# Optimization experiments

Measured on AMD Instinct MI355X. Metric: run time of the kernel, lower is better.

Reference implementation:

```python
import jax, jax.numpy as jnp
import numpy as np

VOCAB = 32000
H = 256
B = 4
S = 512


def setup_inputs() -> dict:
    key = jax.random.key(0)
    ks = jax.random.split(key, 12)
    s = 1.0 / np.sqrt(H)
    inp = {
        "x": jax.random.randint(ks[0], (B, S), 0, VOCAB),
        "embed": jax.random.normal(ks[1], (VOCAB, H), jnp.float32) * 0.02,
        "Wi": jax.random.normal(ks[2], (H, H), jnp.float32) * s,   # i2h weight (in,out)
        "bi": jax.random.normal(ks[3], (H,), jnp.float32) * s,
        "Wh": jax.random.normal(ks[4], (H, H), jnp.float32) * s,   # h2h weight
        "bh": jax.random.normal(ks[5], (H,), jnp.float32) * s,
        "Wa": jax.random.normal(ks[6], (2 * H, H), jnp.float32) * s,  # attn_W (in=2H,out=H)
        "ba": jax.random.normal(ks[7], (H,), jnp.float32) * s,
        "va": jax.random.normal(ks[8], (H,), jnp.float32) * s,     # attn_v (no bias)
        "Wo": jax.random.normal(ks[9], (H, VOCAB), jnp.float32) * s,  # fc_out
        "bo": jax.random.normal(ks[10], (VOCAB,), jnp.float32) * s,
    }
    return inp


def _forward(x, embed, Wi, bi, Wh, bh, Wa, ba, va, Wo, bo):
    emb = embed[x]                               # [B,S,H]
    h0 = jnp.zeros((x.shape[0], H), emb.dtype)

    def step(h, e_t):
        h_new = jnp.tanh(e_t @ Wi + bi + h @ Wh + bh)
        return h_new, h_new

    _, hs = jax.lax.scan(step, h0, jnp.swapaxes(emb, 0, 1))  # [S,B,H]
    enc = jnp.swapaxes(hs, 0, 1)                 # [B,S,H] encoder states

    # Additive attention: energy(t,s) = tanh(W[ h_t ; h_s ] + b), score = v . energy
    Wq, Wk = Wa[:H], Wa[H:]
    q = enc @ Wq                                 # [B,S,H] (query = h_t half)
    k = enc @ Wk                                 # [B,S,H] (history half)
    energy = jnp.tanh(q[:, :, None, :] + k[:, None, :, :] + ba)  # [B,T,S,H]
    scores = jnp.einsum("btsh,h->bts", energy, va)

    seq = x.shape[1]
    causal = jnp.arange(seq)[None, :] < jnp.arange(seq)[:, None]  # [T,S]: s < t strictly
    weights = jax.nn.softmax(jnp.where(causal[None], scores, -1e9), axis=-1)
    ctx = jnp.einsum("bts,bsh->bth", weights, enc)               # [B,S,H]
    # t == 0: context = h_0 itself (no history)
    ctx = jnp.where((jnp.arange(seq) == 0)[None, :, None], enc[:, 0:1, :], ctx)

    out = (ctx + enc) @ Wo + bo                  # [B,S,V]
    return out, enc[:, -1, :]


def reference(x, embed, Wi, bi, Wh, bh, Wa, ba, va, Wo, bo):
    return _forward(x, embed, Wi, bi, Wh, bh, Wa, ba, va, Wo, bo)
```

## Files before the change

kernel.cpp:

```cpp
#include <hip/hip_runtime.h>
#include <hip/hip_bf16.h>
#include <hip/hip_fp16.h>

#define VOCAB 32000
#define H 256
#define B 4
#define S 512

typedef _Float16 f16x8 __attribute__((ext_vector_type(8)));
typedef short s16x8 __attribute__((ext_vector_type(8)));
typedef float f32x4 __attribute__((ext_vector_type(4)));

__device__ __forceinline__ float tanh_fast(float x) {
    float e = exp2f(x * 2.885390081777927f);
    return 1.0f - 2.0f * __builtin_amdgcn_rcpf(e + 1.0f);
}

__device__ __forceinline__ size_t fragIdx(int row, int h) {
    return ((size_t)((((row >> 4) * 8 + (h >> 5)) * 64) + ((h >> 3) & 3) * 16 + (row & 15)) << 3)
           + (h & 7);
}

__global__ __launch_bounds__(256) void k_wot(const float* __restrict__ Wo,
                                             ushort* __restrict__ WoTF) {
    __shared__ float tile[256][65];
    int n0 = blockIdx.x * 64;
    int tx = threadIdx.x & 63, ty = threadIdx.x >> 6;
#pragma unroll
    for (int i = 0; i < 64; ++i) {
        int k = i * 4 + ty;
        tile[k][tx] = Wo[(size_t)k * VOCAB + n0 + tx];
    }
    __syncthreads();
#pragma unroll
    for (int r = 0; r < 8; ++r) {
        int lin = threadIdx.x + 256 * r;
        int ll = lin & 15, lg = (lin >> 4) & 3, kk = (lin >> 6) & 7, nt = lin >> 9;
        int n = nt * 16 + ll;
        s16x8 v;
#pragma unroll
        for (int e = 0; e < 8; ++e) {
            __hip_bfloat16 b = __float2bfloat16(tile[kk * 32 + lg * 8 + e][n]);
            v[e] = *(short*)&b;
        }
        size_t unit = (size_t)(((n0 >> 4) + nt) * 8 + kk) * 64 + lg * 16 + ll;
        *(s16x8*)&WoTF[unit * 8] = v;
    }
}

__global__ void k_eprep(const int* __restrict__ x, const float* __restrict__ embed,
                        const float* __restrict__ Wi, const float* __restrict__ bi,
                        const float* __restrict__ bh, float* __restrict__ Ew) {
    int t = blockIdx.x, j = threadIdx.x;
    __shared__ float es[B][H];
    __shared__ int xs[B];
    if (j < B) xs[j] = x[j * S + t];
    __syncthreads();
    for (int b = 0; b < B; ++b) es[b][j] = embed[(size_t)xs[b] * H + j];
    float bias = bi[j] + bh[j];
    float a0 = bias, a1 = bias, a2 = bias, a3 = bias;
    __syncthreads();
    for (int i = 0; i < H; ++i) {
        float w = Wi[i * H + j];
        a0 += es[0][i] * w; a1 += es[1][i] * w;
        a2 += es[2][i] * w; a3 += es[3][i] * w;
    }
    f32x4 v; v[0] = a0; v[1] = a1; v[2] = a2; v[3] = a3;
    *(f32x4*)&Ew[(t * H + j) * 4] = v;
}

__global__ __launch_bounds__(256, 1) void k_rnn(const float* __restrict__ Ew,
                                                const float* __restrict__ Wh,
                                                _Float16* __restrict__ enc16,
                                                float* __restrict__ out_tail) {
    const int tid = threadIdx.x;
    const int w = tid >> 6;
    const int l = tid & 63;
    const int lg = l >> 4;
    const int ll = l & 15;

    __shared__ _Float16 hbuf[2][4][258];
    for (int idx = tid; idx < 2 * 4 * 258; idx += 256) (&hbuf[0][0][0])[idx] = (_Float16)0.f;

    f16x8 Bf[4][8];
#pragma unroll
    for (int nt = 0; nt < 4; ++nt) {
        int col = w * 64 + nt * 16 + ll;
#pragma unroll
        for (int kk = 0; kk < 8; ++kk) {
            int kb = kk * 32 + lg * 8;
            f16x8 v;
#pragma unroll
            for (int e = 0; e < 8; ++e) v[e] = (_Float16)Wh[(kb + e) * H + col];
            Bf[nt][kk] = v;
        }
    }
    __syncthreads();

    f32x4 eacc[2][4];
#pragma unroll
    for (int d = 0; d < 2; ++d)
#pragma unroll
        for (int nt = 0; nt < 4; ++nt) {
            int j = w * 64 + nt * 16 + ll;
            eacc[d][nt] = *(const f32x4*)&Ew[(d * H + j) * 4];
        }

    const int jcol = w * 64 + lg * 16 + ll;

    for (int t0 = 0; t0 < S; t0 += 2) {
#pragma unroll
        for (int u = 0; u < 2; ++u) {
            const int t = t0 + u;
            const int cur = u, nxt = u ^ 1;

            f16x8 Af[8];
#pragma unroll
            for (int kk = 0; kk < 8; ++kk)
                Af[kk] = *(const f16x8*)&hbuf[cur][l & 3][kk * 32 + lg * 8];

            f32x4 acc[4];
#pragma unroll
            for (int nt = 0; nt < 4; ++nt) acc[nt] = eacc[u][nt];

            {
                int tp = (t + 2 < S) ? t + 2 : S - 1;
#pragma unroll
                for (int nt = 0; nt < 4; ++nt) {
                    int j = w * 64 + nt * 16 + ll;
                    eacc[u][nt] = *(const f32x4*)&Ew[(tp * H + j) * 4];
                }
            }

#pragma unroll
            for (int kk = 0; kk < 8; ++kk)
#pragma unroll
                for (int nt = 0; nt < 4; ++nt)
                    acc[nt] = __builtin_amdgcn_mfma_f32_16x16x32_f16(Af[kk], Bf[nt][kk], acc[nt], 0, 0, 0);

            float v[4];
#pragma unroll
            for (int nt = 0; nt < 4; ++nt) {
                if (lg == nt) {
#pragma unroll
                    for (int r = 0; r < 4; ++r) v[r] = acc[nt][r];
                }
            }

            float hv[4];
#pragma unroll
            for (int r = 0; r < 4; ++r) hv[r] = tanh_fast(v[r]);

#pragma unroll
            for (int r = 0; r < 4; ++r) {
                _Float16 h16 = (_Float16)hv[r];
                hbuf[nxt][r][jcol] = h16;
                enc16[(r * S + t) * H + jcol] = h16;
            }
            if (t == S - 1) {
#pragma unroll
                for (int r = 0; r < 4; ++r) out_tail[r * H + jcol] = hv[r];
            }

            asm volatile("s_waitcnt lgkmcnt(0)" ::: "memory");
            __builtin_amdgcn_s_barrier();
            asm volatile("" ::: "memory");
        }
    }
}

__global__ void k_qk(const _Float16* __restrict__ enc16, const float* __restrict__ Wa,
                     const float* __restrict__ ba, float* __restrict__ q,
                     float* __restrict__ kT, ushort* __restrict__ encF) {
    int r0 = blockIdx.x * 8;
    int j = threadIdx.x;
    __shared__ float es[8][H];
#pragma unroll
    for (int r = 0; r < 8; ++r) es[r][j] = (float)enc16[(r0 + r) * H + j];
    __syncthreads();
    float aq[8] = {0, 0, 0, 0, 0, 0, 0, 0};
    float ak[8] = {0, 0, 0, 0, 0, 0, 0, 0};
    for (int i = 0; i < H; ++i) {
        float wq = Wa[i * H + j];
        float wk = Wa[(H + i) * H + j];
#pragma unroll
        for (int r = 0; r < 8; ++r) { aq[r] += es[r][i] * wq; ak[r] += es[r][i] * wk; }
    }
    float bav = ba[j];
#pragma unroll
    for (int r = 0; r < 8; ++r) {
        int row = r0 + r;
        int b = row >> 9, t = row & (S - 1);
        q[row * H + j] = aq[r];
        kT[((b * H + j) << 9) + t] = ak[r] + bav;
        _Float16 ev = (_Float16)es[r][j];
        size_t unit = (size_t)((b * 16 + (j >> 4)) * 16 + (t >> 5)) * 64 + ((t >> 3) & 3) * 16 + (j & 15);
        encF[unit * 8 + (t & 7)] = *(ushort*)&ev;
    }
}

__global__ void k_attn(const float* __restrict__ q, const float* __restrict__ kT,
                       const float* __restrict__ va, ushort* __restrict__ WgtF) {
    int bt = blockIdx.x;
    int b = bt >> 9, t = bt & (S - 1);
    int tid = threadIdx.x;
    if (t == 0) {
        for (int ss = tid; ss < S; ss += 256) {
            _Float16 hw = (_Float16)((ss == 0) ? 1.f : 0.f);
            size_t unit = (size_t)((b * 32 + (t >> 4)) * 16 + (ss >> 5)) * 64 + ((ss >> 3) & 3) * 16 + (t & 15);
            WgtF[unit * 8 + (ss & 7)] = *(ushort*)&hw;
        }
        return;
    }
    __shared__ float qs[H], vas[H], part[4][S], wgt[S], red[8];
    qs[tid] = q[bt * H + tid];
    vas[tid] = va[tid];
    __syncthreads();

    int sl = tid & 63, g = tid >> 6;
    int nchunk = (t + 63) >> 6;
    const float* kTb = kT + ((size_t)(b * H) << 9);
    for (int c = 0; c < nchunk; ++c) {
        int s = c * 64 + sl;
        float p = 0.f;
        if (s < t) {
            int hb = g * 64;
            for (int i = 0; i < 64; ++i) {
                int h = hb + i;
                p += vas[h] * tanh_fast(qs[h] + kTb[(h << 9) + s]);
            }
        }
        part[g][s] = p;
    }
    __syncthreads();

    float m = -1e30f;
    for (int s = tid; s < t; s += 256) {
        float sc = part[0][s] + part[1][s] + part[2][s] + part[3][s];
        wgt[s] = sc;
        m = fmaxf(m, sc);
    }
#pragma unroll
    for (int off = 32; off; off >>= 1) m = fmaxf(m, __shfl_xor(m, off));
    if ((tid & 63) == 0) red[g] = m;
    __syncthreads();
    m = fmaxf(fmaxf(red[0], red[1]), fmaxf(red[2], red[3]));
    float ssum = 0.f;
    for (int s = tid; s < t; s += 256) {
        float e = exp2f((wgt[s] - m) * 1.4426950408889634f);
        wgt[s] = e;
        ssum += e;
    }
#pragma unroll
    for (int off = 32; off; off >>= 1) ssum += __shfl_xor(ssum, off);
    if ((tid & 63) == 0) red[4 + g] = ssum;
    __syncthreads();
    float inv = 1.0f / (red[4] + red[5] + red[6] + red[7]);

    for (int ss = tid; ss < S; ss += 256) {
        float wv = (ss < t) ? wgt[ss] * inv : 0.f;
        _Float16 hw = (_Float16)wv;
        size_t unit = (size_t)((b * 32 + (t >> 4)) * 16 + (ss >> 5)) * 64 + ((ss >> 3) & 3) * 16 + (t & 15);
        WgtF[unit * 8 + (ss & 7)] = *(ushort*)&hw;
    }
}

__global__ __launch_bounds__(256) void k_ctx(const ushort* __restrict__ WgtF,
                                             const ushort* __restrict__ encF,
                                             const _Float16* __restrict__ enc16,
                                             ushort* __restrict__ AbfF) {
    int b = blockIdx.y;
    int m0 = blockIdx.x * 32;
    int tid = threadIdx.x;
    int wv = tid >> 6, l = tid & 63;
    int lg = l >> 4, ll = l & 15;

    f32x4 acc[2][4];
#pragma unroll
    for (int mt = 0; mt < 2; ++mt)
#pragma unroll
        for (int nt = 0; nt < 4; ++nt) { f32x4 z; z[0]=0.f; z[1]=0.f; z[2]=0.f; z[3]=0.f; acc[mt][nt] = z; }

#pragma unroll
    for (int kk = 0; kk < 16; ++kk) {
        f16x8 a[2], bf[4];
#pragma unroll
        for (int mt = 0; mt < 2; ++mt)
            a[mt] = *(const f16x8*)&WgtF[((size_t)((b * 32 + (m0 >> 4) + mt) * 16 + kk) * 64 + l) * 8];
#pragma unroll
        for (int nt = 0; nt < 4; ++nt)
            bf[nt] = *(const f16x8*)&encF[((size_t)((b * 16 + wv * 4 + nt) * 16 + kk) * 64 + l) * 8];
#pragma unroll
        for (int mt = 0; mt < 2; ++mt)
#pragma unroll
            for (int nt = 0; nt < 4; ++nt)
                acc[mt][nt] = __builtin_amdgcn_mfma_f32_16x16x32_f16(a[mt], bf[nt], acc[mt][nt], 0, 0, 0);
    }

#pragma unroll
    for (int mt = 0; mt < 2; ++mt)
#pragma unroll
        for (int nt = 0; nt < 4; ++nt)
#pragma unroll
            for (int r = 0; r < 4; ++r) {
                int trow = m0 + mt * 16 + lg * 4 + r;
                int h = wv * 64 + nt * 16 + ll;
                float ev = (float)enc16[(size_t)(b * S + trow) * H + h];
                __hip_bfloat16 o = __float2bfloat16(acc[mt][nt][r] + ev);
                AbfF[fragIdx(b * S + trow, h)] = *(ushort*)&o;
            }
}

__global__ __launch_bounds__(256) void k_out(const ushort* __restrict__ AbfF,
                                             const ushort* __restrict__ WoTF,
                                             const float* __restrict__ bo,
                                             float* __restrict__ out) {
    int tid = threadIdx.x;
    int wv = tid >> 6, l = tid & 63;
    int mw = wv >> 1, nw = wv & 1;
    int lg = l >> 4, ll = l & 15;
    int m0 = blockIdx.x * 128 + mw * 64;
    int n0 = blockIdx.y * 128 + nw * 64;

    f32x4 acc[4][4];
#pragma unroll
    for (int mt = 0; mt < 4; ++mt)
#pragma unroll
        for (int nt = 0; nt < 4; ++nt) { f32x4 z; z[0]=0.f; z[1]=0.f; z[2]=0.f; z[3]=0.f; acc[mt][nt] = z; }

#pragma unroll
    for (int kk = 0; kk < 8; ++kk) {
        s16x8 a[4], bf[4];
#pragma unroll
        for (int mt = 0; mt < 4; ++mt)
            a[mt] = *(const s16x8*)&AbfF[((size_t)(((m0 >> 4) + mt) * 8 + kk) * 64 + l) * 8];
#pragma unroll
        for (int nt = 0; nt < 4; ++nt)
            bf[nt] = *(const s16x8*)&WoTF[((size_t)(((n0 >> 4) + nt) * 8 + kk) * 64 + l) * 8];
#pragma unroll
        for (int mt = 0; mt < 4; ++mt)
#pragma unroll
            for (int nt = 0; nt < 4; ++nt)
                acc[mt][nt] = __builtin_amdgcn_mfma_f32_16x16x32_bf16(a[mt], bf[nt], acc[mt][nt], 0, 0, 0);
    }

#pragma unroll
    for (int nt = 0; nt < 4; ++nt) {
        int n = n0 + nt * 16 + ll;
        float bov = bo[n];
#pragma unroll
        for (int mt = 0; mt < 4; ++mt) {
#pragma unroll
            for (int r = 0; r < 4; ++r) {
                int mrow = m0 + mt * 16 + lg * 4 + r;
                out[(size_t)mrow * VOCAB + n] = acc[mt][nt][r] + bov;
            }
        }
    }
}

extern "C" void kernel_launch(void* const* d_in, const int* in_sizes, int n_in,
                              void* d_out, int out_size, void* d_ws, size_t ws_size,
                              hipStream_t stream) {
    const int*   x     = (const int*)d_in[0];
    const float* embed = (const float*)d_in[1];
    const float* Wi    = (const float*)d_in[2];
    const float* bi    = (const float*)d_in[3];
    const float* Wh    = (const float*)d_in[4];
    const float* bh    = (const float*)d_in[5];
    const float* Wa    = (const float*)d_in[6];
    const float* ba    = (const float*)d_in[7];
    const float* va    = (const float*)d_in[8];
    const float* Wo    = (const float*)d_in[9];
    const float* bo    = (const float*)d_in[10];
    float* out = (float*)d_out;

    char* wsb = (char*)d_ws;
    float*    Ew    = (float*)(wsb);
    _Float16* enc16 = (_Float16*)(wsb + (2 << 20));
    float*    q     = (float*)(wsb + (3 << 20));
    float*    kT    = (float*)(wsb + (5 << 20));
    ushort*   AbfF  = (ushort*)(wsb + (7 << 20));
    ushort*   WoTF  = (ushort*)(wsb + (8 << 20));
    ushort*   WgtF  = (ushort*)(wsb + (24 << 20));
    ushort*   encF  = (ushort*)(wsb + (26 << 20));
    float* out_tail = out + (size_t)B * S * VOCAB;

    hipLaunchKernelGGL(k_wot,   dim3(VOCAB / 64),     dim3(256), 0, stream, Wo, WoTF);
    hipLaunchKernelGGL(k_eprep, dim3(S),              dim3(256), 0, stream, x, embed, Wi, bi, bh, Ew);
    hipLaunchKernelGGL(k_rnn,   dim3(1),              dim3(256), 0, stream, Ew, Wh, enc16, out_tail);
    hipLaunchKernelGGL(k_qk,    dim3(B * S / 8),      dim3(256), 0, stream, enc16, Wa, ba, q, kT, encF);
    hipLaunchKernelGGL(k_attn,  dim3(B * S),          dim3(256), 0, stream, q, kT, va, WgtF);
    hipLaunchKernelGGL(k_ctx,   dim3(S / 32, B),      dim3(256), 0, stream, WgtF, encF, enc16, AbfF);
    hipLaunchKernelGGL(k_out,   dim3(16, VOCAB / 128), dim3(256), 0, stream, AbfF, WoTF, bo, out);
}
```

Before: 601.9 us.

## Overlap Wo transpose with serial RNN and keep idle CUs busy until RNN ends

Merges the Wo transpose/bf16 conversion kernel into the single-block RNN launch. Block 0 runs the recurrence while 255 other blocks transpose Wo concurrently. After that, those blocks run a dependent-FMA spin loop until block 0 sets a global flag, presumably to keep the device busy and clocks high during the serial phase. This removes a separate launch and hides the transpose behind the RNN, at the cost of extra power draw and reliance on all blocks being co-resident.

```diff
diff --git a/kernel.cpp b/kernel.cpp
--- a/kernel.cpp
+++ b/kernel.cpp
@@ -19,33 +19,6 @@
 __device__ __forceinline__ size_t fragIdx(int row, int h) {
     return ((size_t)((((row >> 4) * 8 + (h >> 5)) * 64) + ((h >> 3) & 3) * 16 + (row & 15)) << 3)
            + (h & 7);
-}
-
-__global__ __launch_bounds__(256) void k_wot(const float* __restrict__ Wo,
-                                             ushort* __restrict__ WoTF) {
-    __shared__ float tile[256][65];
-    int n0 = blockIdx.x * 64;
-    int tx = threadIdx.x & 63, ty = threadIdx.x >> 6;
-#pragma unroll
-    for (int i = 0; i < 64; ++i) {
-        int k = i * 4 + ty;
-        tile[k][tx] = Wo[(size_t)k * VOCAB + n0 + tx];
-    }
-    __syncthreads();
-#pragma unroll
-    for (int r = 0; r < 8; ++r) {
-        int lin = threadIdx.x + 256 * r;
-        int ll = lin & 15, lg = (lin >> 4) & 3, kk = (lin >> 6) & 7, nt = lin >> 9;
-        int n = nt * 16 + ll;
-        s16x8 v;
-#pragma unroll
-        for (int e = 0; e < 8; ++e) {
-            __hip_bfloat16 b = __float2bfloat16(tile[kk * 32 + lg * 8 + e][n]);
-            v[e] = *(short*)&b;
-        }
-        size_t unit = (size_t)(((n0 >> 4) + nt) * 8 + kk) * 64 + lg * 16 + ll;
-        *(s16x8*)&WoTF[unit * 8] = v;
-    }
 }
 
 __global__ void k_eprep(const int* __restrict__ x, const float* __restrict__ embed,
@@ -69,102 +42,153 @@
     *(f32x4*)&Ew[(t * H + j) * 4] = v;
 }
 
-__global__ __launch_bounds__(256, 1) void k_rnn(const float* __restrict__ Ew,
-                                                const float* __restrict__ Wh,
-                                                _Float16* __restrict__ enc16,
-                                                float* __restrict__ out_tail) {
+__global__ __launch_bounds__(256, 1) void k_rnn_heat(const float* __restrict__ Ew,
+                                                     const float* __restrict__ Wh,
+                                                     const float* __restrict__ Wo,
+                                                     ushort* __restrict__ WoTF,
+                                                     _Float16* __restrict__ enc16,
+                                                     float* __restrict__ out_tail,
+                                                     int* __restrict__ flag) {
+    __shared__ char smem[256 * 81 * 4];
+    const int bid = blockIdx.x;
     const int tid = threadIdx.x;
-    const int w = tid >> 6;
-    const int l = tid & 63;
-    const int lg = l >> 4;
-    const int ll = l & 15;
-
-    __shared__ _Float16 hbuf[2][4][258];
-    for (int idx = tid; idx < 2 * 4 * 258; idx += 256) (&hbuf[0][0][0])[idx] = (_Float16)0.f;
-
-    f16x8 Bf[4][8];
-#pragma unroll
-    for (int nt = 0; nt < 4; ++nt) {
-        int col = w * 64 + nt * 16 + ll;
-#pragma unroll
-        for (int kk = 0; kk < 8; ++kk) {
-            int kb = kk * 32 + lg * 8;
-            f16x8 v;
-#pragma unroll
-            for (int e = 0; e < 8; ++e) v[e] = (_Float16)Wh[(kb + e) * H + col];
-            Bf[nt][kk] = v;
-        }
-    }
-    __syncthreads();
-
-    f32x4 eacc[2][4];
-#pragma unroll
-    for (int d = 0; d < 2; ++d)
+
+    if (bid == 0) {
+        if (tid == 0) __hip_atomic_store(flag, 0, __ATOMIC_RELEASE, __HIP_MEMORY_SCOPE_AGENT);
+        _Float16 (*hbuf)[4][258] = (_Float16(*)[4][258])smem;
+
+        const int w = tid >> 6;
+        const int l = tid & 63;
+        const int lg = l >> 4;
+        const int ll = l & 15;
+
+        for (int idx = tid; idx < 2 * 4 * 258; idx += 256) (&hbuf[0][0][0])[idx] = (_Float16)0.f;
+
+        f16x8 Bf[4][8];
 #pragma unroll
         for (int nt = 0; nt < 4; ++nt) {
-            int j = w * 64 + nt * 16 + ll;
-            eacc[d][nt] = *(const f32x4*)&Ew[(d * H + j) * 4];
-        }
-
-    const int jcol = w * 64 + lg * 16 + ll;
-
-    for (int t0 = 0; t0 < S; t0 += 2) {
-#pragma unroll
-        for (int u = 0; u < 2; ++u) {
-            const int t = t0 + u;
-            const int cur = u, nxt = u ^ 1;
-
-            f16x8 Af[8];
-#pragma unroll
-            for (int kk = 0; kk < 8; ++kk)
-                Af[kk] = *(const f16x8*)&hbuf[cur][l & 3][kk * 32 + lg * 8];
-
-            f32x4 acc[4];
-#pragma unroll
-            for (int nt = 0; nt < 4; ++nt) acc[nt] = eacc[u][nt];
-
-            {
-                int tp = (t + 2 < S) ? t + 2 : S - 1;
+            int col = w * 64 + nt * 16 + ll;
+#pragma unroll
+            for (int kk = 0; kk < 8; ++kk) {
+                int kb = kk * 32 + lg * 8;
+                f16x8 v;
+#pragma unroll
+                for (int e = 0; e < 8; ++e) v[e] = (_Float16)Wh[(kb + e) * H + col];
+                Bf[nt][kk] = v;
+            }
+        }
+        __syncthreads();
+
+        f32x4 eacc[2][4];
+#pragma unroll
+        for (int d = 0; d < 2; ++d)
+#pragma unroll
+            for (int nt = 0; nt < 4; ++nt) {
+                int j = w * 64 + nt * 16 + ll;
+                eacc[d][nt] = *(const f32x4*)&Ew[(d * H + j) * 4];
+            }
+
+        const int jcol = w * 64 + lg * 16 + ll;
+
+        for (int t0 = 0; t0 < S; t0 += 2) {
+#pragma unroll
+            for (int u = 0; u < 2; ++u) {
+                const int t = t0 + u;
+                const int cur = u, nxt = u ^ 1;
+
+                f16x8 Af[8];
+#pragma unroll
+                for (int kk = 0; kk < 8; ++kk)
+                    Af[kk] = *(const f16x8*)&hbuf[cur][l & 3][kk * 32 + lg * 8];
+
+                f32x4 acc[4];
+#pragma unroll
+                for (int nt = 0; nt < 4; ++nt) acc[nt] = eacc[u][nt];
+
+                {
+                    int tp = (t + 2 < S) ? t + 2 : S - 1;
+#pragma unroll
+                    for (int nt = 0; nt < 4; ++nt) {
+                        int j = w * 64 + nt * 16 + ll;
+                        eacc[u][nt] = *(const f32x4*)&Ew[(tp * H + j) * 4];
+                    }
+                }
+
+#pragma unroll
+                for (int kk = 0; kk < 8; ++kk)
+#pragma unroll
+                    for (int nt = 0; nt < 4; ++nt)
+                        acc[nt] = __builtin_amdgcn_mfma_f32_16x16x32_f16(Af[kk], Bf[nt][kk], acc[nt], 0, 0, 0);
+
+                float v[4];
 #pragma unroll
                 for (int nt = 0; nt < 4; ++nt) {
-                    int j = w * 64 + nt * 16 + ll;
-                    eacc[u][nt] = *(const f32x4*)&Ew[(tp * H + j) * 4];
+                    if (lg == nt) {
+#pragma unroll
+                        for (int r = 0; r < 4; ++r) v[r] = acc[nt][r];
+                    }
                 }
-            }
-
-#pragma unroll
-            for (int kk = 0; kk < 8; ++kk)
-#pragma unroll
-                for (int nt = 0; nt < 4; ++nt)
-                    acc[nt] = __builtin_amdgcn_mfma_f32_16x16x32_f16(Af[kk], Bf[nt][kk], acc[nt], 0, 0, 0);
-
-            float v[4];
-#pragma unroll
-            for (int nt = 0; nt < 4; ++nt) {
-                if (lg == nt) {
-#pragma unroll
-                    for (int r = 0; r < 4; ++r) v[r] = acc[nt][r];
+
+                float hv[4];
+#pragma unroll
+                for (int r = 0; r < 4; ++r) hv[r] = tanh_fast(v[r]);
+
+#pragma unroll
+                for (int r = 0; r < 4; ++r) {
+                    _Float16 h16 = (_Float16)hv[r];
+                    hbuf[nxt][r][jcol] = h16;
+                    enc16[(r * S + t) * H + jcol] = h16;
                 }
-            }
-
-            float hv[4];
-#pragma unroll
-            for (int r = 0; r < 4; ++r) hv[r] = tanh_fast(v[r]);
-
-#pragma unroll
-            for (int r = 0; r < 4; ++r) {
-                _Float16 h16 = (_Float16)hv[r];
-                hbuf[nxt][r][jcol] = h16;
-                enc16[(r * S + t) * H + jcol] = h16;
-            }
-            if (t == S - 1) {
-#pragma unroll
-                for (int r = 0; r < 4; ++r) out_tail[r * H + jcol] = hv[r];
-            }
-
-            asm volatile("s_waitcnt lgkmcnt(0)" ::: "memory");
-            __builtin_amdgcn_s_barrier();
-            asm volatile("" ::: "memory");
+                if (t == S - 1) {
+#pragma unroll
+                    for (int r = 0; r < 4; ++r) out_tail[r * H + jcol] = hv[r];
+                }
+
+                asm volatile("s_waitcnt lgkmcnt(0)" ::: "memory");
+                __builtin_amdgcn_s_barrier();
+                asm volatile("" ::: "memory");
+            }
+        }
+        if (tid == 0) __hip_atomic_store(flag, 1, __ATOMIC_RELEASE, __HIP_MEMORY_SCOPE_AGENT);
+    } else {
+        float (*tile)[81] = (float(*)[81])smem;
+        int tx = tid & 63, ty = tid >> 6;
+        for (int job = bid - 1; job < 500; job += 255) {
+            int n0 = job * 64;
+#pragma unroll
+            for (int i = 0; i < 64; ++i) {
+                int k = i * 4 + ty;
+                tile[k][tx] = Wo[(size_t)k * VOCAB + n0 + tx];
+            }
+            __syncthreads();
+#pragma unroll
+            for (int r = 0; r < 8; ++r) {
+                int lin = tid + 256 * r;
+                int ll = lin & 15, lg = (lin >> 4) & 3, kk = (lin >> 6) & 7, nt = lin >> 9;
+                int n = nt * 16 + ll;
+                s16x8 v;
+#pragma unroll
+                for (int e = 0; e < 8; ++e) {
+                    __hip_bfloat16 b = __float2bfloat16(tile[kk * 32 + lg * 8 + e][n]);
+                    v[e] = *(short*)&b;
+                }
+                size_t unit = (size_t)(((n0 >> 4) + nt) * 8 + kk) * 64 + lg * 16 + ll;
+                *(s16x8*)&WoTF[unit * 8] = v;
+            }
+            __syncthreads();
+        }
+        float c0 = 1.0f + (float)tid * 1e-6f, c1 = 2.0f - (float)tid * 1e-6f;
+        const float a = 0.99999988f, b2 = 1e-7f;
+        for (int chunk = 0; chunk < 1024; ++chunk) {
+            for (int i = 0; i < 2048; ++i) {
+                c0 = __builtin_fmaf(c0, a, b2);
+                c1 = __builtin_fmaf(c1, a, b2);
+            }
+            asm volatile("" :: "v"(c0), "v"(c1));
+            if (chunk >= 2) {
+                if (__hip_atomic_load(flag, __ATOMIC_RELAXED, __HIP_MEMORY_SCOPE_AGENT) != 0)
+                    break;
+            }
         }
     }
 }
@@ -384,13 +408,13 @@
     ushort*   WoTF  = (ushort*)(wsb + (8 << 20));
     ushort*   WgtF  = (ushort*)(wsb + (24 << 20));
     ushort*   encF  = (ushort*)(wsb + (26 << 20));
+    int*      flag  = (int*)(wsb + (27 << 20));
     float* out_tail = out + (size_t)B * S * VOCAB;
 
-    hipLaunchKernelGGL(k_wot,   dim3(VOCAB / 64),     dim3(256), 0, stream, Wo, WoTF);
-    hipLaunchKernelGGL(k_eprep, dim3(S),              dim3(256), 0, stream, x, embed, Wi, bi, bh, Ew);
-    hipLaunchKernelGGL(k_rnn,   dim3(1),              dim3(256), 0, stream, Ew, Wh, enc16, out_tail);
-    hipLaunchKernelGGL(k_qk,    dim3(B * S / 8),      dim3(256), 0, stream, enc16, Wa, ba, q, kT, encF);
-    hipLaunchKernelGGL(k_attn,  dim3(B * S),          dim3(256), 0, stream, q, kT, va, WgtF);
-    hipLaunchKernelGGL(k_ctx,   dim3(S / 32, B),      dim3(256), 0, stream, WgtF, encF, enc16, AbfF);
-    hipLaunchKernelGGL(k_out,   dim3(16, VOCAB / 128), dim3(256), 0, stream, AbfF, WoTF, bo, out);
-}
+    hipLaunchKernelGGL(k_eprep,    dim3(S),          dim3(256), 0, stream, x, embed, Wi, bi, bh, Ew);
+    hipLaunchKernelGGL(k_rnn_heat, dim3(256),        dim3(256), 0, stream, Ew, Wh, Wo, WoTF, enc16, out_tail, flag);
+    hipLaunchKernelGGL(k_qk,       dim3(B * S / 8),  dim3(256), 0, stream, enc16, Wa, ba, q, kT, encF);
+    hipLaunchKernelGGL(k_attn,     dim3(B * S),      dim3(256), 0, stream, q, kT, va, WgtF);
+    hipLaunchKernelGGL(k_ctx,      dim3(S / 32, B),  dim3(256), 0, stream, WgtF, encF, enc16, AbfF);
+    hipLaunchKernelGGL(k_out,      dim3(16, VOCAB / 128), dim3(256), 0, stream, AbfF, WoTF, bo, out);
+}
```

Result: slower. 889.7 us (+47.8%).
